# Performance work log

Hardware: AMD Instinct MI355X
Metric: run time of the kernel (lower is better)

## Reference

```python
import jax, jax.numpy as jnp
import numpy as np

NUM_DIM = 2
N, P, Q, C = 2048, 2048, 64, 2

def _mlp(x, layers, activate_final):
    n = len(layers)
    for i, (w, b) in enumerate(layers):
        x = x @ w + b
        if i < n - 1 or activate_final:
            x = jnp.tanh(x)
    return x

def setup_inputs() -> dict:
    key = jax.random.key(0)
    ks = jax.random.split(key, 24)
    s = 0.3  # param scale for numerical sanity
    return {
        "phase_coords": jax.random.normal(ks[0], (N, 2 * NUM_DIM), jnp.float32),
        "boundary_coords": jax.random.normal(ks[1], (N, 2 * NUM_DIM), jnp.float32),
        "coeff_position": jax.random.normal(ks[2], (P, NUM_DIM), jnp.float32),
        "coeff_values": jax.random.uniform(ks[3], (P, C), jnp.float32),
        "scattering_kernel_coords": jax.random.normal(ks[4], (Q, NUM_DIM), jnp.float32),
        "scattering_kernel": jax.random.uniform(ks[5], (Q,), jnp.float32),
        "velocity_weights": jax.random.uniform(ks[6], (Q,), jnp.float32) / Q,
        "attn_w1": s * jax.random.normal(ks[7], (6, 32), jnp.float32),
        "attn_b1": jnp.zeros((32,), jnp.float32),
        "attn_w2": s * jax.random.normal(ks[8], (32, 32), jnp.float32),
        "attn_b2": jnp.zeros((32,), jnp.float32),
        "attn_w3": s * jax.random.normal(ks[9], (32, 1), jnp.float32),
        "attn_b3": jnp.zeros((1,), jnp.float32),
        "green_w1": s * jax.random.normal(ks[10], (4 * NUM_DIM + C, 64), jnp.float32),
        "green_b1": jnp.zeros((64,), jnp.float32),
        "green_w2": s * jax.random.normal(ks[11], (64, 64), jnp.float32),
        "green_b2": jnp.zeros((64,), jnp.float32),
        "green_w3": s * jax.random.normal(ks[12], (64, 64), jnp.float32),
        "green_b3": jnp.zeros((64,), jnp.float32),
        "res_w": s * jax.random.normal(ks[13], (64, 64), jnp.float32),
        "res_b": jnp.zeros((64,), jnp.float32),
        "final_w": s * jax.random.normal(ks[14], (64, 1), jnp.float32),
        "final_b": jnp.zeros((1,), jnp.float32),
    }

def reference(phase_coords, boundary_coords, coeff_position, coeff_values,
              scattering_kernel_coords, scattering_kernel, velocity_weights,
              attn_w1, attn_b1, attn_w2, attn_b2, attn_w3, attn_b3,
              green_w1, green_b1, green_w2, green_b2, green_w3, green_b3,
              res_w, res_b, final_w, final_b):
    attn_layers = [(attn_w1, attn_b1), (attn_w2, attn_b2), (attn_w3, attn_b3)]
    green_layers = [(green_w1, green_b1), (green_w2, green_b2), (green_w3, green_b3)]

    x, v = phase_coords[:, :NUM_DIM], phase_coords[:, NUM_DIM:]     # (N,2),(N,2)
    xp, vp = boundary_coords[:, :NUM_DIM], boundary_coords[:, NUM_DIM:]

    # --- CoefficientNet: MLP attention logits + geometric mask + softmax over P ---
    ang = v / jnp.sqrt(jnp.sum(v**2, -1, keepdims=True) + 1e-16)     # (N,2)
    rel = x[:, None, :] - coeff_position[None, :, :]                 # (N,P,2)
    dist = jnp.sqrt(jnp.sum(rel**2, -1) + 1e-16)                     # (N,P)
    pos_loc = jnp.einsum('npd,nd->np', rel, ang)                     # (N,P)
    ang_loc = pos_loc / (dist + 1e-8)
    frames = jnp.stack([ang_loc, pos_loc], -1)                       # (N,P,2)
    coords = jnp.concatenate([x, v], -1)                             # (N,4)
    qk = jnp.concatenate(
        [jnp.broadcast_to(coords[:, None, :], (coords.shape[0], frames.shape[1], coords.shape[1])), frames], -1)  # (N,P,6)
    logits = _mlp(qk, attn_layers, False)[..., 0]                    # (N,P)
    logits = jnp.where(pos_loc > 0, logits, -1e30)
    aw = jax.nn.softmax(logits, axis=-1)
    coeff = jnp.exp(-(aw @ coeff_values))                            # (N,C)

    # --- GreenFunctionBlock (coefficients only depend on (x,v)) ---
    g0 = jnp.exp(_mlp(jnp.concatenate([x, v, xp, vp, coeff], -1), green_layers, True))  # (N,64)

    # --- res block depth=1: quadrature over velocity_prime (argnum=3) ---
    w_quad = (1.0 - scattering_kernel) * velocity_weights            # (Q,)
    Nn = x.shape[0]; Qq = scattering_kernel_coords.shape[0]
    base = jnp.concatenate([x, v, xp], -1)                           # (N,6)
    inp_q = jnp.concatenate([
        jnp.broadcast_to(base[:, None, :], (Nn, Qq, base.shape[1])),
        jnp.broadcast_to(scattering_kernel_coords[None, :, :], (Nn, Qq, NUM_DIM)),
        jnp.broadcast_to(coeff[:, None, :], (Nn, Qq, coeff.shape[1])),
    ], -1)                                                           # (N,Q,10)
    gq = jnp.exp(_mlp(inp_q, green_layers, True))                    # (N,Q,64)
    quad = jnp.einsum('nqh,q->nh', gq, w_quad)                       # (N,64)
    res = jnp.tanh(quad @ res_w + res_b)                             # widths[-1:], activate_final
    out = g0 + res
    return out @ final_w + final_b                                   # (N,1)
```

## Files before the change

kernel.cpp:

```cpp
#include <hip/hip_runtime.h>

#define NN 2048
#define PP 2048
#define QQ 64
#define GR_ROWS 4
#define GR_SLOTS 80
#define GR_MT 5

typedef __attribute__((ext_vector_type(8))) short short8;
typedef __attribute__((ext_vector_type(4))) float f32x4;
typedef __attribute__((ext_vector_type(4))) unsigned u32x4;

union V4 { u32x4 u; short8 s; };

#if __has_builtin(__builtin_amdgcn_exp2f)
#define EXP2(x) __builtin_amdgcn_exp2f(x)
#else
#define EXP2(x) exp2f(x)
#endif

__device__ __forceinline__ float fast_rcp(float x) { return __builtin_amdgcn_rcpf(x); }

__device__ __forceinline__ float fast_tanh(float x) {
    float t = EXP2(x * 2.885390082f);
    return 1.0f - 2.0f * __builtin_amdgcn_rcpf(t + 1.0f);
}

__device__ __forceinline__ unsigned cvt_pk_bf16(float lo, float hi) {
    unsigned r;
    asm("v_cvt_pk_bf16_f32 %0, %1, %2" : "=v"(r) : "v"(lo), "v"(hi));
    return r;
}
__device__ __forceinline__ unsigned short bf16_bits(float f) {
    unsigned u = __builtin_bit_cast(unsigned, f);
    u += 0x7FFFu + ((u >> 16) & 1u);
    return (unsigned short)(u >> 16);
}
__device__ __forceinline__ float bf16_lo(unsigned pk) {
    return __builtin_bit_cast(float, pk << 16);
}
__device__ __forceinline__ float bf16_hi(unsigned pk) {
    return __builtin_bit_cast(float, pk & 0xFFFF0000u);
}

__global__ __launch_bounds__(512) void attn_kernel(
    const float* __restrict__ pc, const float* __restrict__ cp,
    const float* __restrict__ cv,
    const float* __restrict__ w1, const float* __restrict__ b1,
    const float* __restrict__ w2, const float* __restrict__ b2,
    const float* __restrict__ w3, const float* __restrict__ b3,
    float* __restrict__ coeff_out)
{
    __shared__ unsigned sap[8][528];
    __shared__ unsigned short sidx[8][528];
    __shared__ float sred[24];

    const int t = threadIdx.x;
    const int w = t >> 6, lane = t & 63;
    const int c15 = lane & 15, kg = lane >> 4;
    const int k0 = kg * 8;
    const int n  = blockIdx.x * 2 + (w >> 2);
    const int p0 = (w & 3) * 512;

    const float b3v = b3[0];
    const float x0 = pc[n*4+0], x1 = pc[n*4+1];
    const float v0 = pc[n*4+2], v1 = pc[n*4+3];
    const float rinv = __builtin_amdgcn_rsqf(v0*v0 + v1*v1 + 1e-16f);
    const float a0 = v0 * rinv, a1 = v1 * rinv;

    int cnt = 0;
    #pragma unroll
    for (int i = 0; i < 8; ++i) {
        const int p = p0 + i*64 + lane;
        const float2 cpp = ((const float2*)cp)[p];
        const float r0 = x0 - cpp.x;
        const float r1 = x1 - cpp.y;
        const float pos = fmaf(r0, a0, r1*a1);
        const bool f = pos > 0.0f;
        const unsigned long long mask = __ballot(f);
        if (f) {
            const int idx = cnt + __popcll(mask & ((1ull << lane) - 1ull));
            const float dist = sqrtf(r0*r0 + r1*r1 + 1e-16f);
            const float angl = pos * fast_rcp(dist + 1e-8f);
            sap[w][idx]  = cvt_pk_bf16(angl, pos);
            sidx[w][idx] = (unsigned short)p;
        }
        cnt += __popcll(mask);
    }
    if (lane < 16) {
        sap[w][cnt + lane]  = 0u;
        sidx[w][cnt + lane] = 0;
    }

    union BF { short8 s8; unsigned u[4]; } B0, B1;
    #pragma unroll
    for (int j2 = 0; j2 < 4; ++j2) {
        const int ka = k0 + 2*j2, kb = ka + 1;
        B0.u[j2] = cvt_pk_bf16(w2[ka*32 + c15],      w2[kb*32 + c15]);
        B1.u[j2] = cvt_pk_bf16(w2[ka*32 + c15 + 16], w2[kb*32 + c15 + 16]);
    }
    float b2a[4], b2b[4], w3a[4], w3b[4];
    #pragma unroll
    for (int r = 0; r < 4; ++r) {
        b2a[r] = b2[kg*4 + r];      b2b[r] = b2[16 + kg*4 + r];
        w3a[r] = w3[kg*4 + r];      w3b[r] = w3[16 + kg*4 + r];
    }
    float cfrag[8], w1a[8], w1b[8];
    #pragma unroll
    for (int j = 0; j < 8; ++j) {
        const int k = k0 + j;
        float c = b1[k];
        c = fmaf(x0, w1[0*32+k], c);
        c = fmaf(x1, w1[1*32+k], c);
        c = fmaf(v0, w1[2*32+k], c);
        c = fmaf(v1, w1[3*32+k], c);
        cfrag[j] = c;
        w1a[j] = w1[4*32+k];
        w1b[j] = w1[5*32+k];
    }
    float sw3 = 0.0f;
    #pragma unroll
    for (int j = 0; j < 32; ++j) sw3 += fabsf(w3[j]);
    const float Lb = fabsf(b3v) + sw3;
    const float C_E = (b3v - Lb) * 1.44269504f;

    float s = 0.0f, q0 = 0.0f, q1 = 0.0f;
    const int nt = (cnt + 15) >> 4;
    #pragma unroll 2
    for (int tile = 0; tile < nt; ++tile) {
        const int li = tile*16 + c15;
        const unsigned pk = sap[w][li];
        const float angl = bf16_lo(pk), pos = bf16_hi(pk);

        float pre[8], h[8];
        #pragma unroll
        for (int j = 0; j < 8; ++j)
            pre[j] = fmaf(angl, w1a[j], fmaf(pos, w1b[j], cfrag[j]));
        #pragma unroll
        for (int j = 0; j < 8; ++j) h[j] = fast_tanh(pre[j]);

        union AF { short8 s8; unsigned u[4]; } H;
        #pragma unroll
        for (int j2 = 0; j2 < 4; ++j2)
            H.u[j2] = cvt_pk_bf16(h[2*j2], h[2*j2+1]);

        f32x4 acca = {b2a[0], b2a[1], b2a[2], b2a[3]};
        f32x4 accb = {b2b[0], b2b[1], b2b[2], b2b[3]};
        acca = __builtin_amdgcn_mfma_f32_16x16x32_bf16(B0.s8, H.s8, acca, 0, 0, 0);
        accb = __builtin_amdgcn_mfma_f32_16x16x32_bf16(B1.s8, H.s8, accb, 0, 0, 0);

        float lg = 0.0f;
        #pragma unroll
        for (int r = 0; r < 4; ++r) {
            lg = fmaf(fast_tanh(acca[r]), w3a[r], lg);
            lg = fmaf(fast_tanh(accb[r]), w3b[r], lg);
        }
        lg += __shfl_xor(lg, 16);
        lg += __shfl_xor(lg, 32);

        const bool val = (kg == 0) && (li < cnt);
        const int pidx = (int)sidx[w][li];
        const float2 cvv = ((const float2*)cv)[pidx];
        const float e = val ? EXP2(fmaf(lg, 1.44269504f, C_E)) : 0.0f;
        s += e;
        q0 = fmaf(e, cvv.x, q0);
        q1 = fmaf(e, cvv.y, q1);
    }

    #pragma unroll
    for (int off = 1; off < 64; off <<= 1) {
        s  += __shfl_xor(s, off);
        q0 += __shfl_xor(q0, off);
        q1 += __shfl_xor(q1, off);
    }
    if (lane == 0) {
        sred[w*3 + 0] = s;
        sred[w*3 + 1] = q0;
        sred[w*3 + 2] = q1;
    }
    __syncthreads();
    if (lane == 0 && (w == 0 || w == 4)) {
        float S = 0.0f, Q0 = 0.0f, Q1 = 0.0f;
        #pragma unroll
        for (int i = 0; i < 4; ++i) {
            S  += sred[(w + i)*3 + 0];
            Q0 += sred[(w + i)*3 + 1];
            Q1 += sred[(w + i)*3 + 2];
        }
        if (!(S > 0.0f)) {
            S = (float)PP; Q0 = 0.0f; Q1 = 0.0f;
            for (int p = 0; p < PP; ++p) { Q0 += cv[2*p]; Q1 += cv[2*p+1]; }
        }
        const float invS = fast_rcp(S);
        coeff_out[n*2+0] = __expf(-Q0 * invS);
        coeff_out[n*2+1] = __expf(-Q1 * invS);
    }
}

__global__ __launch_bounds__(256) void green_kernel(
    const float* __restrict__ pc,  const float* __restrict__ bc,
    const float* __restrict__ skc, const float* __restrict__ sk,
    const float* __restrict__ vw,
    const float* __restrict__ gw1, const float* __restrict__ gb1,
    const float* __restrict__ gw2, const float* __restrict__ gb2,
    const float* __restrict__ gw3, const float* __restrict__ gb3,
    const float* __restrict__ rw,  const float* __restrict__ rb,
    const float* __restrict__ fw,  const float* __restrict__ fb,
    const float* __restrict__ coeff,
    float* __restrict__ out)
{
    __shared__ unsigned short sinA[GR_ROWS*GR_SLOTS*16];
    __shared__ unsigned short shb[4][16*64];
    __shared__ float swq[GR_SLOTS];
    __shared__ float sg0[4][64];
    __shared__ float squad[4][64];

    const int t = threadIdx.x;
    const int w = t >> 6, lane = t & 63;
    const int c15 = lane & 15, kg = lane >> 4;
    const int n0 = blockIdx.x * GR_ROWS;

    V4 Bw1[4], Bw2[2][4], Bw3[2][4];
    #pragma unroll
    for (int nt = 0; nt < 4; ++nt) {
        const int col = c15 + nt*16;
        #pragma unroll
        for (int j2 = 0; j2 < 4; ++j2) {
            const int ka = kg*8 + 2*j2, kb = ka + 1;
            const float va = (ka < 10) ? gw1[ka*64 + col] : 0.0f;
            const float vb = (kb < 10) ? gw1[kb*64 + col] : 0.0f;
            Bw1[nt].u[j2] = cvt_pk_bf16(va, vb);
        }
        #pragma unroll
        for (int kt = 0; kt < 2; ++kt) {
            #pragma unroll
            for (int j2 = 0; j2 < 4; ++j2) {
                const int ka = kt*32 + kg*8 + 2*j2, kb = ka + 1;
                Bw2[kt][nt].u[j2] = cvt_pk_bf16(gw2[ka*64 + col], gw2[kb*64 + col]);
                Bw3[kt][nt].u[j2] = cvt_pk_bf16(gw3[ka*64 + col], gw3[kb*64 + col]);
            }
        }
    }
    float b1c[4], b2c[4], b3c[4];
    #pragma unroll
    for (int nt = 0; nt < 4; ++nt) {
        b1c[nt] = gb1[c15 + nt*16];
        b2c[nt] = gb2[c15 + nt*16];
        b3c[nt] = gb3[c15 + nt*16];
    }

    for (int row = t; row < GR_ROWS*GR_SLOTS; row += 256) {
        const int nl = row / GR_SLOTS;
        const int s  = row - nl*GR_SLOTS;
        const int n  = n0 + nl;
        u32x4 lo = {0u,0u,0u,0u}, hi = {0u,0u,0u,0u};
        if (s <= 64) {
            const float X0 = pc[n*4+0], X1 = pc[n*4+1];
            const float V0 = pc[n*4+2], V1 = pc[n*4+3];
            const float XP0 = bc[n*4+0], XP1 = bc[n*4+1];
            float I6, I7;
            if (s == 64) { I6 = bc[n*4+2]; I7 = bc[n*4+3]; }
            else         { I6 = skc[s*2+0]; I7 = skc[s*2+1]; }
            const float C0 = coeff[n*2+0], C1 = coeff[n*2+1];
            lo[0] = cvt_pk_bf16(X0, X1);
            lo[1] = cvt_pk_bf16(V0, V1);
            lo[2] = cvt_pk_bf16(XP0, XP1);
            lo[3] = cvt_pk_bf16(I6, I7);
            hi[0] = cvt_pk_bf16(C0, C1);
        }
        ((u32x4*)sinA)[row*2 + 0] = lo;
        ((u32x4*)sinA)[row*2 + 1] = hi;
    }
    if (t < GR_SLOTS)
        swq[t] = (t < QQ) ? (1.0f - sk[t]) * vw[t] : 0.0f;
    __syncthreads();

    unsigned short* hb = &shb[w][0];
    float qacc[4] = {0.f, 0.f, 0.f, 0.f};

    #pragma unroll 1
    for (int T = 0; T < GR_MT; ++T) {
        const int rm = w*GR_SLOTS + T*16 + c15;
        V4 A1; A1.u = (u32x4){0u,0u,0u,0u};
        if (kg < 2) A1.u = ((u32x4*)sinA)[rm*2 + kg];

        f32x4 acc1[4];
        #pragma unroll
        for (int nt = 0; nt < 4; ++nt) {
            f32x4 a = {b1c[nt], b1c[nt], b1c[nt], b1c[nt]};
            acc1[nt] = __builtin_amdgcn_mfma_f32_16x16x32_bf16(A1.s, Bw1[nt].s, a, 0, 0, 0);
        }
        #pragma unroll
        for (int nt = 0; nt < 4; ++nt) {
            #pragma unroll
            for (int r = 0; r < 4; ++r) {
                const int rl = kg*4 + r;
                hb[rl*64 + ((c15 + nt*16) ^ ((rl&7)<<3))] = bf16_bits(fast_tanh(acc1[nt][r]));
            }
        }
        V4 A2[2];
        #pragma unroll
        for (int kt = 0; kt < 2; ++kt)
            A2[kt].u = ((u32x4*)hb)[(c15*64 + ((kt*32 + kg*8) ^ ((c15&7)<<3))) >> 3];
        f32x4 acc2[4];
        #pragma unroll
        for (int nt = 0; nt < 4; ++nt) {
            f32x4 a = {b2c[nt], b2c[nt], b2c[nt], b2c[nt]};
            a = __builtin_amdgcn_mfma_f32_16x16x32_bf16(A2[0].s, Bw2[0][nt].s, a, 0, 0, 0);
            acc2[nt] = __builtin_amdgcn_mfma_f32_16x16x32_bf16(A2[1].s, Bw2[1][nt].s, a, 0, 0, 0);
        }
        #pragma unroll
        for (int nt = 0; nt < 4; ++nt) {
            #pragma unroll
            for (int r = 0; r < 4; ++r) {
                const int rl = kg*4 + r;
                hb[rl*64 + ((c15 + nt*16) ^ ((rl&7)<<3))] = bf16_bits(fast_tanh(acc2[nt][r]));
            }
        }
        V4 A3[2];
        #pragma unroll
        for (int kt = 0; kt < 2; ++kt)
            A3[kt].u = ((u32x4*)hb)[(c15*64 + ((kt*32 + kg*8) ^ ((c15&7)<<3))) >> 3];
        f32x4 acc3[4];
        #pragma unroll
        for (int nt = 0; nt < 4; ++nt) {
            f32x4 a = {b3c[nt], b3c[nt], b3c[nt], b3c[nt]};
            a = __builtin_amdgcn_mfma_f32_16x16x32_bf16(A3[0].s, Bw3[0][nt].s, a, 0, 0, 0);
            acc3[nt] = __builtin_amdgcn_mfma_f32_16x16x32_bf16(A3[1].s, Bw3[1][nt].s, a, 0, 0, 0);
        }
        #pragma unroll
        for (int r = 0; r < 4; ++r) {
            const int s = T*16 + kg*4 + r;
            const float wq = swq[s];
            #pragma unroll
            for (int nt = 0; nt < 4; ++nt) {
                const float g = __expf(fast_tanh(acc3[nt][r]));
                qacc[nt] = fmaf(wq, g, qacc[nt]);
                if (T == GR_MT-1 && kg == 0 && r == 0) sg0[w][c15 + nt*16] = g;
            }
        }
    }

    #pragma unroll
    for (int nt = 0; nt < 4; ++nt) {
        qacc[nt] += __shfl_xor(qacc[nt], 16);
        qacc[nt] += __shfl_xor(qacc[nt], 32);
    }
    if (kg == 0) {
        #pragma unroll
        for (int nt = 0; nt < 4; ++nt) squad[w][c15 + nt*16] = qacc[nt];
    }

    const int k = lane;
    float r0a = rb[k], r1a = 0.f, r2a = 0.f, r3a = 0.f;
    #pragma unroll
    for (int j = 0; j < 64; j += 4) {
        const float4 qd = *(const float4*)&squad[w][j];
        r0a = fmaf(qd.x, rw[(j+0)*64 + k], r0a);
        r1a = fmaf(qd.y, rw[(j+1)*64 + k], r1a);
        r2a = fmaf(qd.z, rw[(j+2)*64 + k], r2a);
        r3a = fmaf(qd.w, rw[(j+3)*64 + k], r3a);
    }
    const float resv = fast_tanh((r0a + r1a) + (r2a + r3a));
    float term = (sg0[w][k] + resv) * fw[k];
    #pragma unroll
    for (int off = 32; off; off >>= 1) term += __shfl_xor(term, off);
    if (lane == 0) out[n0 + w] = term + fb[0];
}

extern "C" void kernel_launch(void* const* d_in, const int* in_sizes, int n_in,
                              void* d_out, int out_size, void* d_ws, size_t ws_size,
                              hipStream_t stream) {
    const float* pc  = (const float*)d_in[0];
    const float* bc  = (const float*)d_in[1];
    const float* cp  = (const float*)d_in[2];
    const float* cv  = (const float*)d_in[3];
    const float* skc = (const float*)d_in[4];
    const float* sk  = (const float*)d_in[5];
    const float* vw  = (const float*)d_in[6];
    const float* aw1 = (const float*)d_in[7];
    const float* ab1 = (const float*)d_in[8];
    const float* aw2 = (const float*)d_in[9];
    const float* ab2 = (const float*)d_in[10];
    const float* aw3 = (const float*)d_in[11];
    const float* ab3 = (const float*)d_in[12];
    const float* gw1 = (const float*)d_in[13];
    const float* gb1 = (const float*)d_in[14];
    const float* gw2 = (const float*)d_in[15];
    const float* gb2 = (const float*)d_in[16];
    const float* gw3 = (const float*)d_in[17];
    const float* gb3 = (const float*)d_in[18];
    const float* rw  = (const float*)d_in[19];
    const float* rb  = (const float*)d_in[20];
    const float* fw  = (const float*)d_in[21];
    const float* fb  = (const float*)d_in[22];

    float* coeff = (float*)d_ws;
    float* outp  = (float*)d_out;

    attn_kernel<<<NN/2, 512, 0, stream>>>(pc, cp, cv, aw1, ab1, aw2, ab2, aw3, ab3, coeff);
    green_kernel<<<NN/GR_ROWS, 256, 0, stream>>>(pc, bc, skc, sk, vw,
                                                 gw1, gb1, gw2, gb2, gw3, gb3,
                                                 rw, rb, fw, fb, coeff, outp);
}
```

Before: 83.35 us.

## Split attention over P across two blocks per row, finish reduction in green kernel

The attention kernel now launches two blocks per query row, each covering half of the coefficient points, with eight warps of 128 points each instead of two rows per block with 512 points per warp. Each block writes partial sums (S, Q0, Q1) to workspace, and the green kernel combines the two partials, applies the fallback and exp, and stores the coefficients in shared memory. This raises parallelism and shortens per-warp serial work in the attention stage, at the cost of more blocks, a workspace round trip, and an extra sync at the start of the green kernel. Shared buffers shrink to match the smaller per-warp slice.

```diff
diff --git a/kernel.cpp b/kernel.cpp
--- a/kernel.cpp
+++ b/kernel.cpp
@@ -49,18 +49,18 @@
     const float* __restrict__ w1, const float* __restrict__ b1,
     const float* __restrict__ w2, const float* __restrict__ b2,
     const float* __restrict__ w3, const float* __restrict__ b3,
-    float* __restrict__ coeff_out)
+    float4* __restrict__ partials)
 {
-    __shared__ unsigned sap[8][528];
-    __shared__ unsigned short sidx[8][528];
+    __shared__ unsigned sap[8][144];
+    __shared__ unsigned short sidx[8][144];
     __shared__ float sred[24];
 
     const int t = threadIdx.x;
     const int w = t >> 6, lane = t & 63;
     const int c15 = lane & 15, kg = lane >> 4;
     const int k0 = kg * 8;
-    const int n  = blockIdx.x * 2 + (w >> 2);
-    const int p0 = (w & 3) * 512;
+    const int n  = blockIdx.x >> 1;
+    const int p0 = (blockIdx.x & 1) * 1024 + w * 128;
 
     const float b3v = b3[0];
     const float x0 = pc[n*4+0], x1 = pc[n*4+1];
@@ -70,7 +70,7 @@
 
     int cnt = 0;
     #pragma unroll
-    for (int i = 0; i < 8; ++i) {
+    for (int i = 0; i < 2; ++i) {
         const int p = p0 + i*64 + lane;
         const float2 cpp = ((const float2*)cp)[p];
         const float r0 = x0 - cpp.x;
@@ -179,21 +179,15 @@
         sred[w*3 + 2] = q1;
     }
     __syncthreads();
-    if (lane == 0 && (w == 0 || w == 4)) {
+    if (t == 0) {
         float S = 0.0f, Q0 = 0.0f, Q1 = 0.0f;
         #pragma unroll
-        for (int i = 0; i < 4; ++i) {
-            S  += sred[(w + i)*3 + 0];
-            Q0 += sred[(w + i)*3 + 1];
-            Q1 += sred[(w + i)*3 + 2];
-        }
-        if (!(S > 0.0f)) {
-            S = (float)PP; Q0 = 0.0f; Q1 = 0.0f;
-            for (int p = 0; p < PP; ++p) { Q0 += cv[2*p]; Q1 += cv[2*p+1]; }
-        }
-        const float invS = fast_rcp(S);
-        coeff_out[n*2+0] = __expf(-Q0 * invS);
-        coeff_out[n*2+1] = __expf(-Q1 * invS);
+        for (int i = 0; i < 8; ++i) {
+            S  += sred[i*3 + 0];
+            Q0 += sred[i*3 + 1];
+            Q1 += sred[i*3 + 2];
+        }
+        partials[blockIdx.x] = make_float4(S, Q0, Q1, 0.0f);
     }
 }
 
@@ -206,7 +200,8 @@
     const float* __restrict__ gw3, const float* __restrict__ gb3,
     const float* __restrict__ rw,  const float* __restrict__ rb,
     const float* __restrict__ fw,  const float* __restrict__ fb,
-    const float* __restrict__ coeff,
+    const float4* __restrict__ partials,
+    const float* __restrict__ cv,
     float* __restrict__ out)
 {
     __shared__ unsigned short sinA[GR_ROWS*GR_SLOTS*16];
@@ -214,11 +209,31 @@
     __shared__ float swq[GR_SLOTS];
     __shared__ float sg0[4][64];
     __shared__ float squad[4][64];
+    __shared__ float scoef[GR_ROWS][2];
 
     const int t = threadIdx.x;
     const int w = t >> 6, lane = t & 63;
     const int c15 = lane & 15, kg = lane >> 4;
     const int n0 = blockIdx.x * GR_ROWS;
+
+    if (t < 8) {
+        const int row = t >> 1, c = t & 1;
+        const float4 P = partials[(n0 + row)*2 + c];
+        float S = P.x, Q0 = P.y, Q1 = P.z;
+        S  += __shfl_xor(S, 1);
+        Q0 += __shfl_xor(Q0, 1);
+        Q1 += __shfl_xor(Q1, 1);
+        if (c == 0) {
+            if (!(S > 0.0f)) {
+                S = (float)PP; Q0 = 0.0f; Q1 = 0.0f;
+                for (int p = 0; p < PP; ++p) { Q0 += cv[2*p]; Q1 += cv[2*p+1]; }
+            }
+            const float invS = fast_rcp(S);
+            scoef[row][0] = __expf(-Q0 * invS);
+            scoef[row][1] = __expf(-Q1 * invS);
+        }
+    }
+    __syncthreads();
 
     V4 Bw1[4], Bw2[2][4], Bw3[2][4];
     #pragma unroll
@@ -261,7 +276,7 @@
             float I6, I7;
             if (s == 64) { I6 = bc[n*4+2]; I7 = bc[n*4+3]; }
             else         { I6 = skc[s*2+0]; I7 = skc[s*2+1]; }
-            const float C0 = coeff[n*2+0], C1 = coeff[n*2+1];
+            const float C0 = scoef[nl][0], C1 = scoef[nl][1];
             lo[0] = cvt_pk_bf16(X0, X1);
             lo[1] = cvt_pk_bf16(V0, V1);
             lo[2] = cvt_pk_bf16(XP0, XP1);
@@ -395,11 +410,12 @@
     const float* fw  = (const float*)d_in[21];
     const float* fb  = (const float*)d_in[22];
 
-    float* coeff = (float*)d_ws;
-    float* outp  = (float*)d_out;
-
-    attn_kernel<<<NN/2, 512, 0, stream>>>(pc, cp, cv, aw1, ab1, aw2, ab2, aw3, ab3, coeff);
+    float4* partials = (float4*)d_ws;
+    float* outp = (float*)d_out;
+
+    attn_kernel<<<NN*2, 512, 0, stream>>>(pc, cp, cv, aw1, ab1, aw2, ab2, aw3, ab3,
+                                          partials);
     green_kernel<<<NN/GR_ROWS, 256, 0, stream>>>(pc, bc, skc, sk, vw,
                                                  gw1, gb1, gw2, gb2, gw3, gb3,
-                                                 rw, rb, fw, fb, coeff, outp);
-}
+                                                 rw, rb, fw, fb, partials, cv, outp);
+}
```

Measured after the change: 98.80 us. 1.19x slower.
